# Kernel optimization log

Measured on AMD Instinct MI355X. Metric: run time of the kernel, lower is better.

Reference implementation:

```python
import jax, jax.numpy as jnp
import numpy as np

OUT, IN, GROUP = 11008, 4096, 64
NUM_GROUPS = IN // GROUP  # pad = 0 since IN % GROUP == 0


def setup_inputs() -> dict:
    key = jax.random.key(0)
    k_x, k_q, k_s, k_b = jax.random.split(key, 4)
    x = jax.random.normal(k_x, (4, 2048, IN), dtype=jnp.float32)
    # int4 symmetric codes in [-8, 7], stored as int8 like the torch buffer
    qweight = jax.random.randint(k_q, (OUT, NUM_GROUPS, GROUP), -8, 8).astype(jnp.int8)
    # positive per-group scales (amax/7 in the original), stored fp16
    scales = (jax.random.uniform(k_s, (OUT, NUM_GROUPS), dtype=jnp.float32) * 0.02 + 1e-3).astype(jnp.float16)
    bias = (jax.random.normal(k_b, (OUT,), dtype=jnp.float32) * 0.02).astype(jnp.float16)
    return {"x": x, "qweight": qweight, "scales": scales, "bias": bias}


def reference(x, qweight, scales, bias):
    # Fused dequant: w[o, g*GROUP + j] = q[o, g, j] * scales[o, g]
    w = (qweight.astype(jnp.float16) * scales[:, :, None]).reshape(OUT, IN)
    w = w.astype(x.dtype)  # original casts dequantized weight to x.dtype
    # F.linear(x, w, bias): y = x @ w.T + b  -> [B, S, OUT]
    return jnp.einsum('bsi,oi->bso', x, w) + bias.astype(x.dtype)
```

## Files before the change

### kernel.cpp

```cpp
#include <hip/hip_runtime.h>
#include <hip/hip_fp16.h>
#include <stdint.h>


#define M_DIM 8192
#define N_DIM 11008
#define K_DIM 4096
#define MT_TILES 32
#define NT_TILES 43
#define K_TILES 128
#define SLAB 8192

typedef short short8 __attribute__((ext_vector_type(8)));
typedef float floatx4 __attribute__((ext_vector_type(4)));

__device__ __forceinline__ unsigned short f2bf(float f) {
  union { float f; uint32_t u; } c; c.f = f;
  uint32_t u = c.u;
  return (unsigned short)((u + 0x7FFFu + ((u >> 16) & 1u)) >> 16);
}

__device__ __forceinline__ float load_sc(const void* p, size_t idx, bool is_f32) {
  if (is_f32) return ((const float*)p)[idx];
  return __half2float(((const __half*)p)[idx]);
}

__device__ __forceinline__ bool sniff_q_is_i32(const void* qv) {
  const int* w = (const int*)qv;
  bool ok = true;
  #pragma unroll
  for (int j = 0; j < 16; ++j) {
    int v = w[j];
    ok = ok && (v == (int)(signed char)(v & 0xFF));
  }
  return ok;
}
__device__ __forceinline__ bool sniff_s_is_f32(const void* sv) {
  const float* f = (const float*)sv;
  bool ok = true;
  #pragma unroll
  for (int j = 0; j < 8; ++j) {
    float v = f[j];
    ok = ok && (v > 4e-4f) && (v < 6e-2f);
  }
  return ok;
}

__device__ __forceinline__ void gload_lds16(const short* g, short* l) {
  __builtin_amdgcn_global_load_lds(
      (const __attribute__((address_space(1))) uint32_t*)g,
      (__attribute__((address_space(3))) uint32_t*)l, 16, 0, 0);
}

__global__ __launch_bounds__(256)
void prep_fused(const float* __restrict__ x, const void* __restrict__ qv,
                const void* __restrict__ sv,
                short* __restrict__ xh, short* __restrict__ wq) {
  const int tid = threadIdx.x;
  int b = blockIdx.x;

  if (b < NT_TILES * 256) {
    const bool q_is_i32 = sniff_q_is_i32(qv);
    const bool s_is_f32 = sniff_s_is_f32(sv);
    const int nt = b >> 8;
    const int rem = b & 255;
    const int kt = rem >> 1, half = rem & 1;
    const int r = half * 128 + (tid >> 1);
    const int s0 = (tid & 1) * 2;
    const int o = nt * 256 + r;
    const int k0 = kt * 32 + s0 * 8;

    const float s = load_sc(sv, (size_t)o * 64 + (kt >> 1), s_is_f32);

    int codes[16];
    if (q_is_i32) {
      const int* qq = (const int*)qv + (size_t)o * K_DIM + k0;
      #pragma unroll
      for (int j = 0; j < 4; ++j) {
        int4 t = ((const int4*)qq)[j];
        codes[j*4+0]=t.x; codes[j*4+1]=t.y; codes[j*4+2]=t.z; codes[j*4+3]=t.w;
      }
    } else {
      union { int4 v; int8_t c[16]; } u;
      u.v = *(const int4*)((const int8_t*)qv + (size_t)o * K_DIM + k0);
      #pragma unroll
      for (int j = 0; j < 16; ++j) codes[j] = (int)u.c[j];
    }

    short8 h0, h1;
    #pragma unroll
    for (int j = 0; j < 8; ++j) h0[j] = f2bf((float)codes[j] * s);
    #pragma unroll
    for (int j = 0; j < 8; ++j) h1[j] = f2bf((float)codes[8 + j] * s);

    const int w = (r >> 1) & 3;
    short* slab = wq + ((size_t)nt * K_TILES + kt) * SLAB;
    *(short8*)&slab[r * 32 + ((s0    ) ^ w) * 8] = h0;
    *(short8*)&slab[r * 32 + ((s0 + 1) ^ w) * 8] = h1;
  } else {
    b -= NT_TILES * 256;
    const int mt = b >> 8;
    const int rem = b & 255;
    const int kt = rem >> 1, half = rem & 1;
    const int r = half * 128 + (tid >> 1);
    const int s0 = (tid & 1) * 2;
    const int k0 = kt * 32 + s0 * 8;

    const float4* p = (const float4*)(x + (size_t)(mt * 256 + r) * K_DIM + k0);
    float4 f0 = p[0], f1 = p[1], f2 = p[2], f3 = p[3];
    short8 h0, h1;
    h0[0]=f2bf(f0.x); h0[1]=f2bf(f0.y); h0[2]=f2bf(f0.z); h0[3]=f2bf(f0.w);
    h0[4]=f2bf(f1.x); h0[5]=f2bf(f1.y); h0[6]=f2bf(f1.z); h0[7]=f2bf(f1.w);
    h1[0]=f2bf(f2.x); h1[1]=f2bf(f2.y); h1[2]=f2bf(f2.z); h1[3]=f2bf(f2.w);
    h1[4]=f2bf(f3.x); h1[5]=f2bf(f3.y); h1[6]=f2bf(f3.z); h1[7]=f2bf(f3.w);

    const int w = (r >> 1) & 3;
    short* slab = xh + ((size_t)mt * K_TILES + kt) * SLAB;
    *(short8*)&slab[r * 32 + ((s0    ) ^ w) * 8] = h0;
    *(short8*)&slab[r * 32 + ((s0 + 1) ^ w) * 8] = h1;
  }
}

__global__ __launch_bounds__(512)
void gemm8(const short* __restrict__ xh, const short* __restrict__ wq,
           const void* __restrict__ sv, const void* __restrict__ bv,
           float* __restrict__ C) {
  __shared__ __align__(16) short lds[4 * 2 * SLAB];

  const bool s_is_f32 = sniff_s_is_f32(sv);

  const int tid  = threadIdx.x;
  const int lane = tid & 63;
  const int wid  = tid >> 6;
  const int wm = wid >> 2, wn = wid & 3;
  const int lr = lane & 15, lk = lane >> 4;

  const int bid = blockIdx.x;
  const int xcd = bid & 7;
  const int seq = bid >> 3;
  const int nt  = seq >> 2;
  const int mt  = xcd * 4 + (seq & 3);

  const short* Aslab = xh + (size_t)mt * K_TILES * SLAB;
  const short* Bslab = wq + (size_t)nt * K_TILES * SLAB;

  const int swz8 = (lk ^ ((lr >> 1) & 3)) << 3;
  int aoff[8], boff[4];
  #pragma unroll
  for (int mi = 0; mi < 8; ++mi) aoff[mi] = (wm * 128 + mi * 16 + lr) * 32 + swz8;
  #pragma unroll
  for (int ni = 0; ni < 4; ++ni) boff[ni] = (wn * 64 + ni * 16 + lr) * 32 + swz8;

  floatx4 acc[8][4];
  #pragma unroll
  for (int i = 0; i < 8; ++i)
    #pragma unroll
    for (int j = 0; j < 4; ++j)
      acc[i][j] = (floatx4){0.f, 0.f, 0.f, 0.f};

  short8 fa[8], fb[4], ga[8], gb[4];

#define STAGE(t) do {                                                   \
    const short* gA_ = Aslab + (size_t)(t) * SLAB;                      \
    const short* gB_ = Bslab + (size_t)(t) * SLAB;                      \
    short* lA_ = &lds[((t) & 3) * (2 * SLAB)];                          \
    short* lB_ = lA_ + SLAB;                                            \
    gload_lds16(gA_ + tid * 8,        lA_ + tid * 8);                   \
    gload_lds16(gA_ + 4096 + tid * 8, lA_ + 4096 + tid * 8);            \
    gload_lds16(gB_ + tid * 8,        lB_ + tid * 8);                   \
    gload_lds16(gB_ + 4096 + tid * 8, lB_ + 4096 + tid * 8);            \
  } while (0)

#define LOADF(da, db, t) do {                                           \
    const short* lA_ = &lds[((t) & 3) * (2 * SLAB)];                    \
    const short* lB_ = lA_ + SLAB;                                      \
    _Pragma("unroll")                                                   \
    for (int mi = 0; mi < 8; ++mi) da[mi] = *(const short8*)&lA_[aoff[mi]]; \
    _Pragma("unroll")                                                   \
    for (int ni = 0; ni < 4; ++ni) db[ni] = *(const short8*)&lB_[boff[ni]]; \
  } while (0)

#define DOMFMA(sa, sb) do {                                             \
    __builtin_amdgcn_s_setprio(1);                                      \
    _Pragma("unroll")                                                   \
    for (int mi = 0; mi < 8; ++mi)                                      \
      _Pragma("unroll")                                                 \
      for (int ni = 0; ni < 4; ++ni)                                    \
        acc[mi][ni] = __builtin_amdgcn_mfma_f32_16x16x32_bf16(          \
            sa[mi], sb[ni], acc[mi][ni], 0, 0, 0);                      \
    __builtin_amdgcn_s_setprio(0);                                      \
  } while (0)

#define FENCE asm volatile("" ::: "memory")
#define VMCNT(n) asm volatile("s_waitcnt vmcnt(" #n ")" ::: "memory")
#define BARRIER do { FENCE; __builtin_amdgcn_s_barrier(); FENCE; } while (0)

  STAGE(0); STAGE(1);

  for (int kt = 0; kt < K_TILES; kt += 2) {
    VMCNT(0);
    BARRIER;
    if (kt + 2 < K_TILES) {
      STAGE(kt + 2);
      STAGE(kt + 3);
    }
    LOADF(fa, fb, kt);
    LOADF(ga, gb, kt + 1);
    DOMFMA(fa, fb);
    DOMFMA(ga, gb);
  }

#undef STAGE
#undef LOADF
#undef DOMFMA
#undef FENCE
#undef VMCNT
#undef BARRIER

  #pragma unroll
  for (int ni = 0; ni < 4; ++ni) {
    const int col = nt * 256 + wn * 64 + ni * 16 + lr;
    const float bvf = load_sc(bv, (size_t)col, s_is_f32);
    #pragma unroll
    for (int mi = 0; mi < 8; ++mi) {
      const int rbase = mt * 256 + wm * 128 + mi * 16 + lk * 4;
      #pragma unroll
      for (int rr = 0; rr < 4; ++rr)
        C[(size_t)(rbase + rr) * N_DIM + col] = acc[mi][ni][rr] + bvf;
    }
  }
}

__global__ __launch_bounds__(256)
void gemm_fused(const float* __restrict__ x, const void* __restrict__ qv,
                const void* __restrict__ sv, const void* __restrict__ bv,
                float* __restrict__ C) {
  __shared__ __align__(16) short As[128 * 64];
  __shared__ __align__(16) short Bs[128 * 64];

  const bool q_is_i32 = sniff_q_is_i32(qv);
  const bool s_is_f32 = sniff_s_is_f32(sv);

  const int tid  = threadIdx.x;
  const int lane = tid & 63;
  const int wid  = tid >> 6;
  const int wm = wid >> 1, wn = wid & 1;
  const int lr = lane & 15, lk = lane >> 4;

  const int nwg = gridDim.x;
  const int cpx = nwg >> 3;
  const int bid = blockIdx.x;
  const int swz = (bid & 7) * cpx + (bid >> 3);
  const int per_g = 4 * 86;
  const int g = swz / per_g;
  const int r = swz - g * per_g;
  const int mt = (g << 2) + (r & 3);
  const int nt = r >> 2;

  const int row0 = mt * 128;
  const int col0 = nt * 128;

  floatx4 acc[4][4];
  #pragma unroll
  for (int i = 0; i < 4; ++i)
    #pragma unroll
    for (int j = 0; j < 4; ++j)
      acc[i][j] = (floatx4){0.f, 0.f, 0.f, 0.f};

  for (int kt = 0; kt < K_DIM / 64; ++kt) {
    const int k0 = kt * 64;
    #pragma unroll
    for (int i = 0; i < 4; ++i) {
      const int cid = i * 256 + tid;
      const int arow = cid >> 3, ac = (cid & 7) << 3;
      const float4* p = (const float4*)(x + (size_t)(row0 + arow) * K_DIM + k0 + ac);
      float4 a = p[0], b = p[1];
      short8 h;
      h[0]=f2bf(a.x); h[1]=f2bf(a.y); h[2]=f2bf(a.z); h[3]=f2bf(a.w);
      h[4]=f2bf(b.x); h[5]=f2bf(b.y); h[6]=f2bf(b.z); h[7]=f2bf(b.w);
      *(short8*)&As[arow * 64 + ac] = h;
    }
    #pragma unroll
    for (int i = 0; i < 2; ++i) {
      const int cid = i * 256 + tid;
      const int brow = cid >> 2, bc = (cid & 3) << 4;
      const float s = load_sc(sv, (size_t)(col0 + brow) * 64 + kt, s_is_f32);
      int codes[16];
      if (q_is_i32) {
        const int* qq = (const int*)qv + (size_t)(col0 + brow) * K_DIM + k0 + bc;
        #pragma unroll
        for (int j = 0; j < 4; ++j) {
          int4 t = ((const int4*)qq)[j];
          codes[j*4+0]=t.x; codes[j*4+1]=t.y; codes[j*4+2]=t.z; codes[j*4+3]=t.w;
        }
      } else {
        union { int4 v; int8_t c[16]; } u;
        u.v = *(const int4*)((const int8_t*)qv + (size_t)(col0 + brow) * K_DIM + k0 + bc);
        #pragma unroll
        for (int j = 0; j < 16; ++j) codes[j] = (int)u.c[j];
      }
      short8 h0, h1;
      #pragma unroll
      for (int j = 0; j < 8; ++j) h0[j] = f2bf((float)codes[j] * s);
      #pragma unroll
      for (int j = 0; j < 8; ++j) h1[j] = f2bf((float)codes[8 + j] * s);
      *(short8*)&Bs[brow * 64 + bc]     = h0;
      *(short8*)&Bs[brow * 64 + bc + 8] = h1;
    }
    __syncthreads();
    #pragma unroll
    for (int ks = 0; ks < 2; ++ks) {
      short8 a[4], b[4];
      #pragma unroll
      for (int mi = 0; mi < 4; ++mi)
        a[mi] = *(const short8*)&As[(wm * 64 + mi * 16 + lr) * 64 + ks * 32 + lk * 8];
      #pragma unroll
      for (int ni = 0; ni < 4; ++ni)
        b[ni] = *(const short8*)&Bs[(wn * 64 + ni * 16 + lr) * 64 + ks * 32 + lk * 8];
      #pragma unroll
      for (int mi = 0; mi < 4; ++mi)
        #pragma unroll
        for (int ni = 0; ni < 4; ++ni)
          acc[mi][ni] = __builtin_amdgcn_mfma_f32_16x16x32_bf16(
              a[mi], b[ni], acc[mi][ni], 0, 0, 0);
    }
    __syncthreads();
  }

  #pragma unroll
  for (int ni = 0; ni < 4; ++ni) {
    const int col = col0 + wn * 64 + ni * 16 + lr;
    const float bvf = load_sc(bv, (size_t)col, s_is_f32);
    #pragma unroll
    for (int mi = 0; mi < 4; ++mi) {
      const int rbase = row0 + wm * 64 + mi * 16 + lk * 4;
      #pragma unroll
      for (int rr = 0; rr < 4; ++rr)
        C[(size_t)(rbase + rr) * N_DIM + col] = acc[mi][ni][rr] + bvf;
    }
  }
}

extern "C" void kernel_launch(void* const* d_in, const int* in_sizes, int n_in,
                              void* d_out, int out_size, void* d_ws, size_t ws_size,
                              hipStream_t stream) {
  const float* x  = (const float*)d_in[0];
  const void*  q  = (const void*)d_in[1];
  const void*  sc = (const void*)d_in[2];
  const void*  bs = (const void*)d_in[3];
  float* y = (float*)d_out;
  (void)in_sizes; (void)n_in; (void)out_size;

  const size_t xh_bytes = (size_t)M_DIM * K_DIM * 2;
  const size_t wq_bytes = (size_t)N_DIM * K_DIM * 2;

  if (ws_size >= xh_bytes + wq_bytes) {
    short* xh = (short*)d_ws;
    short* wq = (short*)((char*)d_ws + xh_bytes);
    prep_fused<<<NT_TILES * 256 + MT_TILES * 256, dim3(256), 0, stream>>>(
        x, q, sc, xh, wq);
    gemm8<<<MT_TILES * NT_TILES, dim3(512), 0, stream>>>(xh, wq, sc, bs, y);
  } else {
    gemm_fused<<<(M_DIM / 128) * (N_DIM / 128), dim3(256), 0, stream>>>(x, q, sc, bs, y);
  }
}
```

Before: 776.7 us.

## Split main loop into half-tile phases interleaving LDS reads, staging and MFMA

Restructures the GEMM main loop so each k-tile is handled in two halves of the A fragment, using fewer fragment registers, with global-to-LDS staging of A and B split across the phases. It waits with vmcnt(4) rather than draining all loads, so prefetch of the next tiles overlaps compute. The kernel then runs a tail for the last two tiles. The aim is to cut register pressure and hide load latency, at the cost of several extra barriers per k-tile that may serialise the waves.

New measurement: 779.0 us. About the same (+0.3%).

```diff
diff --git a/kernel.cpp b/kernel.cpp
--- a/kernel.cpp
+++ b/kernel.cpp
@@ -145,9 +145,12 @@
   const short* Bslab = wq + (size_t)nt * K_TILES * SLAB;
 
   const int swz8 = (lk ^ ((lr >> 1) & 3)) << 3;
-  int aoff[8], boff[4];
-  #pragma unroll
-  for (int mi = 0; mi < 8; ++mi) aoff[mi] = (wm * 128 + mi * 16 + lr) * 32 + swz8;
+  int aoff[2][4], boff[4];
+  #pragma unroll
+  for (int h = 0; h < 2; ++h)
+    #pragma unroll
+    for (int mi = 0; mi < 4; ++mi)
+      aoff[h][mi] = (wm * 128 + h * 64 + mi * 16 + lr) * 32 + swz8;
   #pragma unroll
   for (int ni = 0; ni < 4; ++ni) boff[ni] = (wn * 64 + ni * 16 + lr) * 32 + swz8;
 
@@ -158,61 +161,104 @@
     for (int j = 0; j < 4; ++j)
       acc[i][j] = (floatx4){0.f, 0.f, 0.f, 0.f};
 
-  short8 fa[8], fb[4], ga[8], gb[4];
-
-#define STAGE(t) do {                                                   \
-    const short* gA_ = Aslab + (size_t)(t) * SLAB;                      \
-    const short* gB_ = Bslab + (size_t)(t) * SLAB;                      \
-    short* lA_ = &lds[((t) & 3) * (2 * SLAB)];                          \
-    short* lB_ = lA_ + SLAB;                                            \
-    gload_lds16(gA_ + tid * 8,        lA_ + tid * 8);                   \
-    gload_lds16(gA_ + 4096 + tid * 8, lA_ + 4096 + tid * 8);            \
-    gload_lds16(gB_ + tid * 8,        lB_ + tid * 8);                   \
-    gload_lds16(gB_ + 4096 + tid * 8, lB_ + 4096 + tid * 8);            \
-  } while (0)
-
-#define LOADF(da, db, t) do {                                           \
-    const short* lA_ = &lds[((t) & 3) * (2 * SLAB)];                    \
-    const short* lB_ = lA_ + SLAB;                                      \
-    _Pragma("unroll")                                                   \
-    for (int mi = 0; mi < 8; ++mi) da[mi] = *(const short8*)&lA_[aoff[mi]]; \
-    _Pragma("unroll")                                                   \
-    for (int ni = 0; ni < 4; ++ni) db[ni] = *(const short8*)&lB_[boff[ni]]; \
-  } while (0)
-
-#define DOMFMA(sa, sb) do {                                             \
-    __builtin_amdgcn_s_setprio(1);                                      \
-    _Pragma("unroll")                                                   \
-    for (int mi = 0; mi < 8; ++mi)                                      \
-      _Pragma("unroll")                                                 \
-      for (int ni = 0; ni < 4; ++ni)                                    \
-        acc[mi][ni] = __builtin_amdgcn_mfma_f32_16x16x32_bf16(          \
-            sa[mi], sb[ni], acc[mi][ni], 0, 0, 0);                      \
-    __builtin_amdgcn_s_setprio(0);                                      \
-  } while (0)
+  short8 fa[4], fb[4];
 
 #define FENCE asm volatile("" ::: "memory")
 #define VMCNT(n) asm volatile("s_waitcnt vmcnt(" #n ")" ::: "memory")
 #define BARRIER do { FENCE; __builtin_amdgcn_s_barrier(); FENCE; } while (0)
 
-  STAGE(0); STAGE(1);
-
-  for (int kt = 0; kt < K_TILES; kt += 2) {
-    VMCNT(0);
-    BARRIER;
-    if (kt + 2 < K_TILES) {
-      STAGE(kt + 2);
-      STAGE(kt + 3);
-    }
-    LOADF(fa, fb, kt);
-    LOADF(ga, gb, kt + 1);
-    DOMFMA(fa, fb);
-    DOMFMA(ga, gb);
-  }
-
-#undef STAGE
-#undef LOADF
-#undef DOMFMA
+#define STAGE_A(t) do {                                                 \
+    const short* gA_ = Aslab + (size_t)(t) * SLAB;                      \
+    short* lA_ = &lds[((t) & 3) * (2 * SLAB)];                          \
+    gload_lds16(gA_ + tid * 8,        lA_ + tid * 8);                   \
+    gload_lds16(gA_ + 4096 + tid * 8, lA_ + 4096 + tid * 8);            \
+    FENCE;                                                              \
+  } while (0)
+
+#define STAGE_B(t) do {                                                 \
+    const short* gB_ = Bslab + (size_t)(t) * SLAB;                      \
+    short* lB_ = &lds[((t) & 3) * (2 * SLAB)] + SLAB;                   \
+    gload_lds16(gB_ + tid * 8,        lB_ + tid * 8);                   \
+    gload_lds16(gB_ + 4096 + tid * 8, lB_ + 4096 + tid * 8);            \
+    FENCE;                                                              \
+  } while (0)
+
+#define LOADA(h, t) do {                                                \
+    const short* lA_ = &lds[((t) & 3) * (2 * SLAB)];                    \
+    _Pragma("unroll")                                                   \
+    for (int mi = 0; mi < 4; ++mi) fa[mi] = *(const short8*)&lA_[aoff[h][mi]]; \
+  } while (0)
+
+#define LOADB(t) do {                                                   \
+    const short* lB_ = &lds[((t) & 3) * (2 * SLAB)] + SLAB;             \
+    _Pragma("unroll")                                                   \
+    for (int ni = 0; ni < 4; ++ni) fb[ni] = *(const short8*)&lB_[boff[ni]]; \
+  } while (0)
+
+#define MFMA_HALF(h) do {                                               \
+    __builtin_amdgcn_s_setprio(1);                                      \
+    _Pragma("unroll")                                                   \
+    for (int mi = 0; mi < 4; ++mi)                                      \
+      _Pragma("unroll")                                                 \
+      for (int ni = 0; ni < 4; ++ni)                                    \
+        acc[(h) * 4 + mi][ni] = __builtin_amdgcn_mfma_f32_16x16x32_bf16( \
+            fa[mi], fb[ni], acc[(h) * 4 + mi][ni], 0, 0, 0);            \
+    __builtin_amdgcn_s_setprio(0);                                      \
+  } while (0)
+
+  STAGE_A(0); STAGE_B(0); STAGE_A(1); STAGE_B(1);
+
+  for (int kt = 0; kt < 126; kt += 2) {
+    VMCNT(4);
+    BARRIER;
+    LOADA(0, kt);
+    LOADB(kt);
+    STAGE_A(kt + 2);
+    BARRIER;
+    MFMA_HALF(0);
+    BARRIER;
+    LOADA(1, kt);
+    STAGE_B(kt + 2);
+    BARRIER;
+    MFMA_HALF(1);
+    VMCNT(4);
+    BARRIER;
+    LOADA(0, kt + 1);
+    LOADB(kt + 1);
+    STAGE_A(kt + 3);
+    BARRIER;
+    MFMA_HALF(0);
+    BARRIER;
+    LOADA(1, kt + 1);
+    STAGE_B(kt + 3);
+    BARRIER;
+    MFMA_HALF(1);
+  }
+
+  VMCNT(4);
+  BARRIER;
+  LOADA(0, 126); LOADB(126);
+  BARRIER;
+  MFMA_HALF(0);
+  BARRIER;
+  LOADA(1, 126);
+  BARRIER;
+  MFMA_HALF(1);
+  VMCNT(0);
+  BARRIER;
+  LOADA(0, 127); LOADB(127);
+  BARRIER;
+  MFMA_HALF(0);
+  BARRIER;
+  LOADA(1, 127);
+  BARRIER;
+  MFMA_HALF(1);
+
+#undef STAGE_A
+#undef STAGE_B
+#undef LOADA
+#undef LOADB
+#undef MFMA_HALF
 #undef FENCE
 #undef VMCNT
 #undef BARRIER
```
